# Optimization experiments

Hardware: AMD Instinct MI355X
Metric: run time of the kernel (lower is better)

The kernel has to match this reference:

```python
import jax, jax.numpy as jnp
import numpy as np

B = 1048576
L = 32

def setup_inputs() -> dict:
    key = jax.random.key(0)
    k1, k2 = jax.random.split(key)
    D_pred_logit = jax.random.normal(k1, (B, L), dtype=jnp.float32)
    # D is a true distribution over L bins: random positives normalized per row
    raw = jax.random.uniform(k2, (B, L), dtype=jnp.float32)
    D = raw / jnp.sum(raw, axis=1, keepdims=True)
    return {"D_pred_logit": D_pred_logit, "D": D}

def reference(D_pred_logit, D):
    Lc = D.shape[1]
    # Ordinal similarity matrix A[j,k] = 1 - |j-k|/(L-1)  (PSD by construction)
    idx = jnp.arange(Lc, dtype=jnp.float32)
    A = 1.0 - jnp.abs(idx[:, None] - idx[None, :]) / (Lc - 1)
    A = A.astype(D.dtype)
    Q = D - jax.nn.softmax(D_pred_logit, axis=1)  # [B, L]
    # mean(diag(Q @ A @ Q^T)) == mean over rows of sum((Q @ A) * Q, axis=1)
    # (same math; avoids the B x B intermediate of the original)
    per_row = jnp.sum((Q @ A) * Q, axis=1)  # [B]
    return jnp.mean(per_row)
```

## Files before the change

### kernel.cpp

```cpp
#include <hip/hip_runtime.h>


#define L_BINS  32
#define NTHREAD 256
#define PAD     36

typedef float vfloat4 __attribute__((ext_vector_type(4)));

__device__ __forceinline__ vfloat4 nt_load4(const float* p) {
    return __builtin_nontemporal_load((const vfloat4*)p);
}

__global__ __launch_bounds__(NTHREAD) void qfd2_main(const float* __restrict__ logit,
                                                     const float* __restrict__ D,
                                                     float* __restrict__ partial) {
    __shared__ float zbuf[NTHREAD * PAD];
    __shared__ float dbuf[NTHREAD * PAD];

    const int t = threadIdx.x;
    const size_t tile_f = (size_t)blockIdx.x * (NTHREAD * L_BINS);
    const float* zg = logit + tile_f;
    const float* dg = D + tile_f;

    vfloat4 vz[8], vd[8];
#pragma unroll
    for (int k = 0; k < 8; ++k) vz[k] = nt_load4(zg + (k * NTHREAD + t) * 4);
#pragma unroll
    for (int k = 0; k < 8; ++k) vd[k] = nt_load4(dg + (k * NTHREAD + t) * 4);
#pragma unroll
    for (int k = 0; k < 8; ++k) {
        const int p = k * NTHREAD + t;
        *(vfloat4*)&zbuf[(p >> 3) * PAD + (p & 7) * 4] = vz[k];
    }
#pragma unroll
    for (int k = 0; k < 8; ++k) {
        const int p = k * NTHREAD + t;
        *(vfloat4*)&dbuf[(p >> 3) * PAD + (p & 7) * 4] = vd[k];
    }
    __syncthreads();

    float z[L_BINS], d[L_BINS];
#pragma unroll
    for (int f = 0; f < 8; ++f) ((vfloat4*)z)[f] = *(const vfloat4*)&zbuf[t * PAD + f * 4];
#pragma unroll
    for (int f = 0; f < 8; ++f) ((vfloat4*)d)[f] = *(const vfloat4*)&dbuf[t * PAD + f * 4];

    float tm[16];
#pragma unroll
    for (int i = 0; i < 16; ++i) tm[i] = fmaxf(z[i], z[i + 16]);
#pragma unroll
    for (int i = 0; i < 8; ++i)  tm[i] = fmaxf(tm[i], tm[i + 8]);
#pragma unroll
    for (int i = 0; i < 4; ++i)  tm[i] = fmaxf(tm[i], tm[i + 4]);
    const float m = fmaxf(fmaxf(tm[0], tm[2]), fmaxf(tm[1], tm[3]));

    float e[L_BINS];
#pragma unroll
    for (int i = 0; i < L_BINS; ++i) e[i] = __expf(z[i] - m);
    float u[16];
#pragma unroll
    for (int i = 0; i < 16; ++i) u[i] = e[i] + e[i + 16];
#pragma unroll
    for (int i = 0; i < 8; ++i)  u[i] = u[i] + u[i + 8];
#pragma unroll
    for (int i = 0; i < 4; ++i)  u[i] = u[i] + u[i + 4];
    const float rs = 1.0f / ((u[0] + u[2]) + (u[1] + u[3]));

    float P = 0.0f, sP = 0.0f, sP2 = 0.0f;
#pragma unroll
    for (int i = 0; i < L_BINS - 1; ++i) {
        P  += d[i] - e[i] * rs;
        sP += P;
        sP2 = fmaf(P, P, sP2);
    }
    P += d[L_BINS - 1] - e[L_BINS - 1] * rs;
    const float S = P;
    float res = (2.0f / 31.0f) * (sP2 - S * sP) + S * S;

#pragma unroll
    for (int msk = 1; msk < 64; msk <<= 1) res += __shfl_xor(res, msk);

    __shared__ float wpart[NTHREAD / 64];
    if ((t & 63) == 0) wpart[t >> 6] = res;
    __syncthreads();
    if (t == 0)
        partial[blockIdx.x] = (wpart[0] + wpart[1]) + (wpart[2] + wpart[3]);
}

__global__ __launch_bounds__(256) void qfd2_fin(const float* __restrict__ partial,
                                                float* __restrict__ out,
                                                int nblocks, int rows) {
    double a = 0.0;
    for (int i = threadIdx.x; i < nblocks; i += 256) a += (double)partial[i];
#pragma unroll
    for (int msk = 1; msk < 64; msk <<= 1) a += __shfl_xor(a, msk);

    __shared__ double wp[4];
    if ((threadIdx.x & 63) == 0) wp[threadIdx.x >> 6] = a;
    __syncthreads();
    if (threadIdx.x == 0)
        out[0] = (float)(((wp[0] + wp[1]) + (wp[2] + wp[3])) / (double)rows);
}

extern "C" void kernel_launch(void* const* d_in, const int* in_sizes, int n_in,
                              void* d_out, int out_size, void* d_ws, size_t ws_size,
                              hipStream_t stream) {
    const float* logit = (const float*)d_in[0];
    const float* D     = (const float*)d_in[1];
    float* out         = (float*)d_out;
    float* partial     = (float*)d_ws;

    const int rows    = in_sizes[0] / L_BINS;
    const int nblocks = rows / NTHREAD;

    qfd2_main<<<nblocks, NTHREAD, 0, stream>>>(logit, D, partial);
    qfd2_fin<<<1, 256, 0, stream>>>(partial, out, nblocks, rows);
}
```

Baseline: 253.0 us.

## Use persistent grid-stride blocks with register prefetch of next tile

Replaces one-block-per-tile launch with a fixed grid of 1024 persistent blocks that loop over tiles, accumulating per-thread results. While computing the current tile, the next tile's logits and targets are loaded into registers to overlap global memory latency with math. This adds an extra barrier per tile and raises register pressure, which may reduce occupancy.

```diff
diff --git a/kernel.cpp b/kernel.cpp
--- a/kernel.cpp
+++ b/kernel.cpp
@@ -4,6 +4,7 @@
 #define L_BINS  32
 #define NTHREAD 256
 #define PAD     36
+#define NBLOCKS 1024
 
 typedef float vfloat4 __attribute__((ext_vector_type(4)));
 
@@ -13,75 +14,93 @@
 
 __global__ __launch_bounds__(NTHREAD) void qfd2_main(const float* __restrict__ logit,
                                                      const float* __restrict__ D,
-                                                     float* __restrict__ partial) {
+                                                     float* __restrict__ partial,
+                                                     int ntiles) {
     __shared__ float zbuf[NTHREAD * PAD];
     __shared__ float dbuf[NTHREAD * PAD];
 
     const int t = threadIdx.x;
-    const size_t tile_f = (size_t)blockIdx.x * (NTHREAD * L_BINS);
-    const float* zg = logit + tile_f;
-    const float* dg = D + tile_f;
+    float acc = 0.0f;
 
     vfloat4 vz[8], vd[8];
+    int g = blockIdx.x;
+
+    if (g < ntiles) {
+        const float* zg = logit + (size_t)g * (NTHREAD * L_BINS);
+        const float* dg = D     + (size_t)g * (NTHREAD * L_BINS);
 #pragma unroll
-    for (int k = 0; k < 8; ++k) vz[k] = nt_load4(zg + (k * NTHREAD + t) * 4);
+        for (int k = 0; k < 8; ++k) vz[k] = nt_load4(zg + (k * NTHREAD + t) * 4);
 #pragma unroll
-    for (int k = 0; k < 8; ++k) vd[k] = nt_load4(dg + (k * NTHREAD + t) * 4);
+        for (int k = 0; k < 8; ++k) vd[k] = nt_load4(dg + (k * NTHREAD + t) * 4);
+    }
+
+    for (; g < ntiles; g += NBLOCKS) {
 #pragma unroll
-    for (int k = 0; k < 8; ++k) {
-        const int p = k * NTHREAD + t;
-        *(vfloat4*)&zbuf[(p >> 3) * PAD + (p & 7) * 4] = vz[k];
-    }
+        for (int k = 0; k < 8; ++k) {
+            const int p = k * NTHREAD + t;
+            *(vfloat4*)&zbuf[(p >> 3) * PAD + (p & 7) * 4] = vz[k];
+        }
 #pragma unroll
-    for (int k = 0; k < 8; ++k) {
-        const int p = k * NTHREAD + t;
-        *(vfloat4*)&dbuf[(p >> 3) * PAD + (p & 7) * 4] = vd[k];
-    }
-    __syncthreads();
+        for (int k = 0; k < 8; ++k) {
+            const int p = k * NTHREAD + t;
+            *(vfloat4*)&dbuf[(p >> 3) * PAD + (p & 7) * 4] = vd[k];
+        }
+        __syncthreads();
 
-    float z[L_BINS], d[L_BINS];
+        float z[L_BINS], d[L_BINS];
 #pragma unroll
-    for (int f = 0; f < 8; ++f) ((vfloat4*)z)[f] = *(const vfloat4*)&zbuf[t * PAD + f * 4];
+        for (int f = 0; f < 8; ++f) ((vfloat4*)z)[f] = *(const vfloat4*)&zbuf[t * PAD + f * 4];
 #pragma unroll
-    for (int f = 0; f < 8; ++f) ((vfloat4*)d)[f] = *(const vfloat4*)&dbuf[t * PAD + f * 4];
+        for (int f = 0; f < 8; ++f) ((vfloat4*)d)[f] = *(const vfloat4*)&dbuf[t * PAD + f * 4];
+        __syncthreads();
 
-    float tm[16];
+        const int gn = g + NBLOCKS;
+        if (gn < ntiles) {
+            const float* zg = logit + (size_t)gn * (NTHREAD * L_BINS);
+            const float* dg = D     + (size_t)gn * (NTHREAD * L_BINS);
 #pragma unroll
-    for (int i = 0; i < 16; ++i) tm[i] = fmaxf(z[i], z[i + 16]);
+            for (int k = 0; k < 8; ++k) vz[k] = nt_load4(zg + (k * NTHREAD + t) * 4);
 #pragma unroll
-    for (int i = 0; i < 8; ++i)  tm[i] = fmaxf(tm[i], tm[i + 8]);
+            for (int k = 0; k < 8; ++k) vd[k] = nt_load4(dg + (k * NTHREAD + t) * 4);
+        }
+
+        float tm[16];
 #pragma unroll
-    for (int i = 0; i < 4; ++i)  tm[i] = fmaxf(tm[i], tm[i + 4]);
-    const float m = fmaxf(fmaxf(tm[0], tm[2]), fmaxf(tm[1], tm[3]));
-
-    float e[L_BINS];
+        for (int i = 0; i < 16; ++i) tm[i] = fmaxf(z[i], z[i + 16]);
 #pragma unroll
-    for (int i = 0; i < L_BINS; ++i) e[i] = __expf(z[i] - m);
-    float u[16];
+        for (int i = 0; i < 8; ++i)  tm[i] = fmaxf(tm[i], tm[i + 8]);
 #pragma unroll
-    for (int i = 0; i < 16; ++i) u[i] = e[i] + e[i + 16];
-#pragma unroll
-    for (int i = 0; i < 8; ++i)  u[i] = u[i] + u[i + 8];
-#pragma unroll
-    for (int i = 0; i < 4; ++i)  u[i] = u[i] + u[i + 4];
-    const float rs = 1.0f / ((u[0] + u[2]) + (u[1] + u[3]));
-
-    float P = 0.0f, sP = 0.0f, sP2 = 0.0f;
-#pragma unroll
-    for (int i = 0; i < L_BINS - 1; ++i) {
-        P  += d[i] - e[i] * rs;
-        sP += P;
-        sP2 = fmaf(P, P, sP2);
-    }
-    P += d[L_BINS - 1] - e[L_BINS - 1] * rs;
-    const float S = P;
-    float res = (2.0f / 31.0f) * (sP2 - S * sP) + S * S;
+        for (int i = 0; i < 4; ++i)  tm[i] = fmaxf(tm[i], tm[i + 4]);
+        const float m = fmaxf(fmaxf(tm[0], tm[2]), fmaxf(tm[1], tm[3]));
 
 #pragma unroll
-    for (int msk = 1; msk < 64; msk <<= 1) res += __shfl_xor(res, msk);
+        for (int i = 0; i < L_BINS; ++i) z[i] = __expf(z[i] - m);
+        float u[16];
+#pragma unroll
+        for (int i = 0; i < 16; ++i) u[i] = z[i] + z[i + 16];
+#pragma unroll
+        for (int i = 0; i < 8; ++i)  u[i] = u[i] + u[i + 8];
+#pragma unroll
+        for (int i = 0; i < 4; ++i)  u[i] = u[i] + u[i + 4];
+        const float rs = 1.0f / ((u[0] + u[2]) + (u[1] + u[3]));
+
+        float P = 0.0f, sP = 0.0f, sP2 = 0.0f;
+#pragma unroll
+        for (int i = 0; i < L_BINS - 1; ++i) {
+            P  += d[i] - z[i] * rs;
+            sP += P;
+            sP2 = fmaf(P, P, sP2);
+        }
+        P += d[L_BINS - 1] - z[L_BINS - 1] * rs;
+        const float S = P;
+        acc += (2.0f / 31.0f) * (sP2 - S * sP) + S * S;
+    }
+
+#pragma unroll
+    for (int msk = 1; msk < 64; msk <<= 1) acc += __shfl_xor(acc, msk);
 
     __shared__ float wpart[NTHREAD / 64];
-    if ((t & 63) == 0) wpart[t >> 6] = res;
+    if ((t & 63) == 0) wpart[t >> 6] = acc;
     __syncthreads();
     if (t == 0)
         partial[blockIdx.x] = (wpart[0] + wpart[1]) + (wpart[2] + wpart[3]);
@@ -110,9 +129,9 @@
     float* out         = (float*)d_out;
     float* partial     = (float*)d_ws;
 
-    const int rows    = in_sizes[0] / L_BINS;
-    const int nblocks = rows / NTHREAD;
+    const int rows   = in_sizes[0] / L_BINS;
+    const int ntiles = rows / NTHREAD;
 
-    qfd2_main<<<nblocks, NTHREAD, 0, stream>>>(logit, D, partial);
-    qfd2_fin<<<1, 256, 0, stream>>>(partial, out, nblocks, rows);
+    qfd2_main<<<NBLOCKS, NTHREAD, 0, stream>>>(logit, D, partial, ntiles);
+    qfd2_fin<<<1, 256, 0, stream>>>(partial, out, NBLOCKS, rows);
 }
```

Measured after the change: 247.3 us. -2.2%, faster.
